# Optimization experiments

Hardware: AMD Instinct MI355X
Metric: run time of the kernel (lower is better)

Reference implementation:

```python
import jax, jax.numpy as jnp
import numpy as np

DIM = 768
HEADS = 12
HEAD_DIM = DIM // HEADS
SCALE = HEAD_DIM ** -0.5
LN_EPS = 1e-5


def setup_inputs() -> dict:
    key = jax.random.key(0)
    ks = jax.random.split(key, 12)
    B, N, C = 8, 1024, DIM
    g = (6.0 / (C + 3 * C)) ** 0.5  # xavier_uniform bound for qkv
    gp = (6.0 / (C + C)) ** 0.5     # xavier_uniform bound for proj
    return {
        "x": jax.random.normal(ks[0], (B, N, C), jnp.float32),
        "w_qkv_id": jax.random.uniform(ks[1], (3 * C, C), jnp.float32, -g, g),
        "w_qkv_cloth": jax.random.uniform(ks[2], (3 * C, C), jnp.float32, -g, g),
        "w_proj_id": jax.random.uniform(ks[3], (C, C), jnp.float32, -gp, gp),
        "b_proj_id": jnp.zeros((C,), jnp.float32),
        "w_proj_cloth": jax.random.uniform(ks[4], (C, C), jnp.float32, -gp, gp),
        "b_proj_cloth": jnp.zeros((C,), jnp.float32),
        "ln_id_w": jnp.ones((C,), jnp.float32),
        "ln_id_b": jnp.zeros((C,), jnp.float32),
        "ln_cloth_w": jnp.ones((C,), jnp.float32),
        "ln_cloth_b": jnp.zeros((C,), jnp.float32),
        "orth_scale": jnp.asarray(0.1, jnp.float32),
    }


def _layernorm(x, w, b):
    mu = jnp.mean(x, axis=-1, keepdims=True)
    var = jnp.var(x, axis=-1, keepdims=True)
    return (x - mu) * jax.lax.rsqrt(var + LN_EPS) * w + b


def _split_heads(qkv, B, N):
    qkv = qkv.reshape(B, N, 3, HEADS, HEAD_DIM).transpose(2, 0, 3, 1, 4)
    return qkv[0], qkv[1], qkv[2]


def _attn(q, k, v):
    s = jnp.einsum("bhnd,bhmd->bhnm", q, k) * SCALE
    s = jnp.clip(s, -20.0, 20.0)
    a = jax.nn.softmax(s, axis=-1)
    a = jnp.where(jnp.isnan(a), jnp.zeros_like(a), a)  # nan guard (dropout = eval/identity)
    return jnp.einsum("bhnm,bhmd->bhnd", a, v)


def reference(x, w_qkv_id, w_qkv_cloth, w_proj_id, b_proj_id, w_proj_cloth,
              b_proj_cloth, ln_id_w, ln_id_b, ln_cloth_w, ln_cloth_b, orth_scale):
    B, N, C = x.shape
    q_id, k_id, v_id = _split_heads(x @ w_qkv_id.T, B, N)
    q_cl, k_cl, v_cl = _split_heads(x @ w_qkv_cloth.T, B, N)

    # Gram-Schmidt orthogonal projection of q_id against q_cloth
    dot = jnp.sum(q_id * q_cl, axis=-1, keepdims=True)          # [B,H,N,1]
    norm_sq = jnp.sum(q_cl * q_cl, axis=-1, keepdims=True) + 1e-5
    coeff = jnp.clip(dot / norm_sq, -1.0, 1.0)
    scale = jnp.clip(orth_scale, 0.0, 1.0)
    q_id_ortho = q_id - scale * (coeff * q_cl)
    saliency = jnp.clip(jnp.mean(jnp.abs(dot) / jnp.sqrt(norm_sq), axis=1), 0.0, 1.0)  # [B,N,1]

    out_id = _attn(q_id_ortho, k_id, v_id).transpose(0, 2, 1, 3).reshape(B, N, C)
    out_cl = _attn(q_cl, k_cl, v_cl).transpose(0, 2, 1, 3).reshape(B, N, C)

    id_feat = _layernorm(out_id @ w_proj_id.T + b_proj_id, ln_id_w, ln_id_b)
    cl_feat = _layernorm(out_cl @ w_proj_cloth.T + b_proj_cloth, ln_cloth_w, ln_cloth_b)
    return id_feat, cl_feat, saliency
```

## Files before the change

### kernel.cpp

```cpp
#include <hip/hip_runtime.h>

typedef unsigned short u16;
typedef short s16x8 __attribute__((ext_vector_type(8)));
typedef float f32x4 __attribute__((ext_vector_type(4)));

#define DEV __device__ __forceinline__

#if __has_builtin(__builtin_amdgcn_exp2f)
#define EXP2F(x) __builtin_amdgcn_exp2f(x)
#else
#define EXP2F(x) exp2f(x)
#endif

DEV u16 f2bf(float f) {
  unsigned int u = __float_as_uint(f);
  u = (u + 0x7fffu + ((u >> 16) & 1u)) >> 16;
  return (u16)u;
}
DEV float bf2f(u16 h) { return __uint_as_float(((unsigned int)h) << 16); }
DEV unsigned int pk_trunc(float lo, float hi) {
  return __builtin_amdgcn_perm(__float_as_uint(hi), __float_as_uint(lo), 0x07060302u);
}

DEV void g2l16(const void* g, void* l) {
  __builtin_amdgcn_global_load_lds(
      (const __attribute__((address_space(1))) unsigned int*)g,
      (__attribute__((address_space(3))) unsigned int*)l, 16, 0, 0);
}

#define SPLANE 6291456

#define BAR __builtin_amdgcn_s_barrier()
#define WAIT_VM(n) asm volatile("s_waitcnt vmcnt(" #n ")" ::: "memory")
#define WAIT_LGKM0 asm volatile("s_waitcnt lgkmcnt(0)" ::: "memory")
#define PRIO1 __builtin_amdgcn_s_setprio(1)
#define PRIO0 __builtin_amdgcn_s_setprio(0)

__global__ __launch_bounds__(256) void k_cvt(const float* __restrict__ x,
                                             const float* __restrict__ wqi,
                                             const float* __restrict__ wqc,
                                             const float* __restrict__ wpi,
                                             const float* __restrict__ wpc,
                                             u16* __restrict__ xb,
                                             u16* __restrict__ wqkv,
                                             u16* __restrict__ wproj) {
  int i = blockIdx.x * 256 + threadIdx.x;
  const float* src; u16* dst; int off;
  if (i < 1572864)      { src = x;   dst = xb;             off = 0; }
  else if (i < 2015232) { src = wqi; dst = wqkv;           off = 1572864; }
  else if (i < 2457600) { src = wqc; dst = wqkv + 1769472; off = 2015232; }
  else if (i < 2605056) { src = wpi; dst = wproj;          off = 2457600; }
  else                  { src = wpc; dst = wproj + 589824; off = 2605056; }
  int j = i - off;
  float4 v = ((const float4*)src)[j];
  ushort4 o;
  o.x = f2bf(v.x); o.y = f2bf(v.y); o.z = f2bf(v.z); o.w = f2bf(v.w);
  ((ushort4*)dst)[j] = o;
}


DEV void qstg(const u16* pX, const u16* pW, int koff, u16* lA, u16* lB, int wave) {
#pragma unroll
  for (int it = 0; it < 4; ++it) {
    int rb = wave * 32 + it * 8;
    g2l16(pX + koff + it * (8 * 768), &lA[rb * 64]);
    g2l16(pW + koff + it * (8 * 768), &lB[rb * 64]);
  }
}

DEV void qcomp(const u16* lA, const u16* lB, int wr, int wc, int fr, int fq,
               f32x4 (&acc)[4][4]) {
#pragma unroll
  for (int ks = 0; ks < 2; ++ks) {
    s16x8 af[4], bfr[4];
#pragma unroll
    for (int i = 0; i < 4; i++) {
      int row = wc + i * 16 + fr;
      af[i] = *(const s16x8*)&lB[row * 64 + (((ks * 4 + fq) ^ (row & 7)) * 8)];
    }
#pragma unroll
    for (int j = 0; j < 4; j++) {
      int row = wr + j * 16 + fr;
      bfr[j] = *(const s16x8*)&lA[row * 64 + (((ks * 4 + fq) ^ (row & 7)) * 8)];
    }
    PRIO1;
#pragma unroll
    for (int i = 0; i < 4; i++)
#pragma unroll
      for (int j = 0; j < 4; j++)
        acc[i][j] = __builtin_amdgcn_mfma_f32_16x16x32_bf16(af[i], bfr[j], acc[i][j], 0, 0, 0);
    PRIO0;
  }
}

__global__ __launch_bounds__(256, 2) void k_qkv_gemm(const u16* __restrict__ X,
                                                     const u16* __restrict__ Wq,
                                                     u16* __restrict__ QK,
                                                     u16* __restrict__ VT,
                                                     float* __restrict__ sal) {
  __shared__ __align__(16) u16 sm[32768];

  const int idx = blockIdx.x;
  const int tid = threadIdx.x;
  if (idx < 32) sal[idx * 256 + tid] = 0.f;

  const int swz = (idx & 7) * 288 + (idx >> 3);
  const int bx = swz % 18;
  const int rem = swz / 18;
  const int by = rem & 63;
  const int z = rem >> 6;
  const int n0 = bx * 128, m0 = by * 128;

  const int wave = tid >> 6, lane = tid & 63;
  const int wr = (wave >> 1) * 64, wc = (wave & 1) * 64;
  const int fr = lane & 15, fq = lane >> 4;

  const int srow = lane >> 3;
  const int scol = ((lane & 7) ^ srow) * 8;

  const u16* pX = X + (size_t)(m0 + wave * 32 + srow) * 768 + scol;
  const u16* pW = Wq + (size_t)z * (2304 * 768) + (size_t)(n0 + wave * 32 + srow) * 768 + scol;

  u16* const lA0 = sm;
  u16* const lB0 = sm + 8192;
  u16* const lA1 = sm + 16384;
  u16* const lB1 = sm + 24576;

  f32x4 acc[4][4];
#pragma unroll
  for (int i = 0; i < 4; i++)
#pragma unroll
    for (int j = 0; j < 4; j++) acc[i][j] = (f32x4){0.f, 0.f, 0.f, 0.f};

  qstg(pX, pW, 0, lA0, lB0, wave);
  qstg(pX, pW, 64, lA1, lB1, wave);
  WAIT_VM(8);
  BAR;

  const u16* pX2 = pX + 128;
  const u16* pW2 = pW + 128;

#pragma unroll
  for (int ii = 0; ii < 6; ++ii) {
    qcomp(lA0, lB0, wr, wc, fr, fq, acc);
    BAR;
    if (ii < 5) {
      qstg(pX2, pW2, 0, lA0, lB0, wave);
      WAIT_VM(8);
    } else {
      WAIT_VM(0);
    }
    BAR;
    qcomp(lA1, lB1, wr, wc, fr, fq, acc);
    BAR;
    if (ii < 5) {
      qstg(pX2, pW2, 64, lA1, lB1, wave);
      WAIT_VM(8);
      pX2 += 128; pW2 += 128;
    }
    BAR;
  }

  __syncthreads();
  const int c0 = n0 + wc;
  const int t0 = m0 + wr;
  const int b = t0 >> 10, tt0 = t0 & 1023;
  if (c0 < 1536) {
    u16* ep = sm + wave * 4608;
#pragma unroll
    for (int i = 0; i < 4; i++)
#pragma unroll
      for (int j = 0; j < 4; j++) {
        unsigned int lo = (unsigned int)f2bf(acc[i][j][0]) | ((unsigned int)f2bf(acc[i][j][1]) << 16);
        unsigned int hi = (unsigned int)f2bf(acc[i][j][2]) | ((unsigned int)f2bf(acc[i][j][3]) << 16);
        uint2 pk; pk.x = lo; pk.y = hi;
        *(uint2*)&ep[(j * 16 + fr) * 72 + i * 16 + fq * 4] = pk;
      }
    __builtin_amdgcn_s_waitcnt(0);
    const int three = (c0 >= 768) ? 1 : 0;
    const int h = (c0 - three * 768) >> 6;
    u16* dst = QK + ((size_t)z * 2 + three) * SPLANE +
               ((size_t)(b * 12 + h) * 1024 + tt0) * 64;
#pragma unroll
    for (int pass = 0; pass < 8; ++pass) {
      int row = pass * 8 + (lane >> 3);
      int dch = (lane & 7) * 8;
      *(uint4*)&dst[(size_t)row * 64 + dch] = *(const uint4*)&ep[row * 72 + dch];
    }
  } else {
    const int h = (c0 - 1536) >> 6;
    u16* dst = VT + (size_t)z * SPLANE + ((size_t)(b * 12 + h) * 64) * 1024 + tt0;
    u16* ep2 = sm + wave * 5632;
#pragma unroll
    for (int i = 0; i < 4; i++)
#pragma unroll
      for (int j = 0; j < 4; j++)
#pragma unroll
        for (int r = 0; r < 4; r++)
          ep2[(i * 16 + fq * 4 + r) * 88 + j * 16 + fr] = f2bf(acc[i][j][r]);
    __builtin_amdgcn_s_waitcnt(0);
#pragma unroll
    for (int pass = 0; pass < 8; ++pass) {
      int d = pass * 8 + (lane >> 3);
      int tch = (lane & 7) * 8;
      *(uint4*)&dst[(size_t)d * 1024 + tch] = *(const uint4*)&ep2[d * 88 + tch];
    }
  }
}

#define AST 72
#define PST 40
__global__ __launch_bounds__(256, 3) void k_attn(const u16* __restrict__ QK,
                                                 const u16* __restrict__ VT,
                                                 const float* __restrict__ orth_scale,
                                                 float* __restrict__ sal,
                                                 u16* __restrict__ aout) {
  __shared__ __align__(16) u16 sm[19456];
  u16* lK = sm;
  u16* lVT = sm + 4608;
  const int lid = blockIdx.x;
  const int swz = (lid & 7) * 96 + (lid >> 3);
  const int qb = swz & 3;
  const int pr = swz >> 2;
  const int z = pr / 96, bh = pr - (pr / 96) * 96;
  const int q0 = qb * 256;
  const int b = bh / 12, hd = bh - b * 12;
  const size_t plane = (size_t)bh * 65536;
  const u16* Q  = QK + (size_t)z * 2 * SPLANE + plane;
  const u16* K  = QK + ((size_t)z * 2 + 1) * SPLANE + plane;
  const u16* Vt = VT + (size_t)z * SPLANE + plane;

  const int tid = threadIdx.x, wave = tid >> 6, lane = tid & 63;
  const int fr = lane & 15, fq = lane >> 4;
  u16* lP = sm + 9216 + wave * 2560;

  s16x8 qf[4][2];
#pragma unroll
  for (int s = 0; s < 4; s++) {
    const u16* qrow = Q + (size_t)(q0 + wave * 64 + s * 16 + fr) * 64;
    qf[s][0] = *(const s16x8*)&qrow[fq * 8];
    qf[s][1] = *(const s16x8*)&qrow[32 + fq * 8];
  }

  if (z == 0) {
    const float scale = fminf(fmaxf(orth_scale[0], 0.f), 1.f);
    const u16* Qc = QK + (size_t)2 * SPLANE + plane;
#pragma unroll
    for (int s = 0; s < 4; s++) {
      const u16* qcrow = Qc + (size_t)(q0 + wave * 64 + s * 16 + fr) * 64;
      s16x8 qc0 = *(const s16x8*)&qcrow[fq * 8];
      s16x8 qc1 = *(const s16x8*)&qcrow[32 + fq * 8];
      float d = 0.f, nq = 0.f;
#pragma unroll
      for (int e = 0; e < 8; e++) {
        float a0 = bf2f((u16)qf[s][0][e]), a1 = bf2f((u16)qf[s][1][e]);
        float c0 = bf2f((u16)qc0[e]),      c1 = bf2f((u16)qc1[e]);
        d  = fmaf(a0, c0, fmaf(a1, c1, d));
        nq = fmaf(c0, c0, fmaf(c1, c1, nq));
      }
      d += __shfl_xor(d, 16);  d += __shfl_xor(d, 32);
      nq += __shfl_xor(nq, 16); nq += __shfl_xor(nq, 32);
      nq += 1e-5f;
      float coeff = fminf(fmaxf(d / nq, -1.f), 1.f);
      float sc = scale * coeff;
#pragma unroll
      for (int e = 0; e < 8; e++) {
        qf[s][0][e] = (short)f2bf(bf2f((u16)qf[s][0][e]) - sc * bf2f((u16)qc0[e]));
        qf[s][1][e] = (short)f2bf(bf2f((u16)qf[s][1][e]) - sc * bf2f((u16)qc1[e]));
      }
      if (lane < 16)
        atomicAdd(&sal[b * 1024 + q0 + wave * 64 + s * 16 + fr], fabsf(d) / sqrtf(nq));
    }
  }

  f32x4 oacc[4][4];
  float lsum[4];
#pragma unroll
  for (int s = 0; s < 4; s++) {
    lsum[s] = 0.f;
#pragma unroll
    for (int j = 0; j < 4; j++) oacc[s][j] = (f32x4){0.f, 0.f, 0.f, 0.f};
  }

  const int srow = tid >> 3, sc8 = (tid & 7) * 8;

  uint4 rk0 = *(const uint4*)&K[(size_t)srow * 64 + sc8];
  uint4 rk1 = *(const uint4*)&K[(size_t)(srow + 32) * 64 + sc8];
  uint4 rv0 = *(const uint4*)&Vt[(size_t)srow * 1024 + sc8];
  uint4 rv1 = *(const uint4*)&Vt[(size_t)(srow + 32) * 1024 + sc8];

  for (int kv0 = 0; kv0 < 1024; kv0 += 64) {
    __syncthreads();
    *(uint4*)&lK[srow * AST + sc8]         = rk0;
    *(uint4*)&lK[(srow + 32) * AST + sc8]  = rk1;
    *(uint4*)&lVT[srow * AST + sc8]        = rv0;
    *(uint4*)&lVT[(srow + 32) * AST + sc8] = rv1;
    __syncthreads();

    {
      int nxt = (kv0 + 64) & 1023;
      const u16* kb = K + (size_t)nxt * 64;
      rk0 = *(const uint4*)&kb[(size_t)srow * 64 + sc8];
      rk1 = *(const uint4*)&kb[(size_t)(srow + 32) * 64 + sc8];
      const u16* vb = Vt + nxt;
      rv0 = *(const uint4*)&vb[(size_t)srow * 1024 + sc8];
      rv1 = *(const uint4*)&vb[(size_t)(srow + 32) * 1024 + sc8];
    }

#pragma unroll
    for (int ph = 0; ph < 2; ++ph) {
#pragma unroll
      for (int jh = 0; jh < 2; ++jh) {
        const int jt = ph * 2 + jh;
        s16x8 kf0 = *(const s16x8*)&lK[(jt * 16 + fr) * AST + fq * 8];
        s16x8 kf1 = *(const s16x8*)&lK[(jt * 16 + fr) * AST + 32 + fq * 8];
#pragma unroll
        for (int s = 0; s < 4; s++) {
          f32x4 t = (f32x4){0.f, 0.f, 0.f, 0.f};
          t = __builtin_amdgcn_mfma_f32_16x16x32_bf16(kf0, qf[s][0], t, 0, 0, 0);
          t = __builtin_amdgcn_mfma_f32_16x16x32_bf16(kf1, qf[s][1], t, 0, 0, 0);
          float p0 = EXP2F(fmaf(t[0], 0.18033688f, -28.8539008f));
          float p1 = EXP2F(fmaf(t[1], 0.18033688f, -28.8539008f));
          float p2 = EXP2F(fmaf(t[2], 0.18033688f, -28.8539008f));
          float p3 = EXP2F(fmaf(t[3], 0.18033688f, -28.8539008f));
          lsum[s] += (p0 + p1) + (p2 + p3);
          uint2 pk; pk.x = pk_trunc(p0, p1); pk.y = pk_trunc(p2, p3);
          *(uint2*)&lP[(s * 16 + fr) * PST + jh * 16 + fq * 4] = pk;
        }
      }
      WAIT_LGKM0;
      s16x8 pa[4];
#pragma unroll
      for (int s = 0; s < 4; s++) pa[s] = *(const s16x8*)&lP[(s * 16 + fr) * PST + fq * 8];
#pragma unroll
      for (int jt = 0; jt < 4; jt++) {
        s16x8 vb = *(const s16x8*)&lVT[(jt * 16 + fr) * AST + ph * 32 + fq * 8];
#pragma unroll
        for (int s = 0; s < 4; s++)
          oacc[s][jt] = __builtin_amdgcn_mfma_f32_16x16x32_bf16(pa[s], vb, oacc[s][jt], 0, 0, 0);
      }
    }
  }

#pragma unroll
  for (int s = 0; s < 4; s++) {
    float v = lsum[s];
    v += __shfl_xor(v, 16);
    v += __shfl_xor(v, 32);
    lsum[s] = v;
  }
#pragma unroll
  for (int s = 0; s < 4; s++) {
#pragma unroll
    for (int r = 0; r < 4; r++) {
      float inv = 1.f / __shfl(lsum[s], fq * 4 + r);
      int t = q0 + wave * 64 + s * 16 + fq * 4 + r;
      size_t base = ((size_t)z * 8192 + b * 1024 + t) * 768 + hd * 64 + fr;
#pragma unroll
      for (int jt = 0; jt < 4; jt++)
        aout[base + jt * 16] = f2bf(oacc[s][jt][r] * inv);
    }
  }
}

__global__ __launch_bounds__(256) void k_proj_gemm(const u16* __restrict__ A,
                                                   const u16* __restrict__ Wp,
                                                   const float* __restrict__ bias_id,
                                                   const float* __restrict__ bias_cl,
                                                   float* __restrict__ sal,
                                                   u16* __restrict__ out) {
  __shared__ __align__(16) u16 sm[18432];
  u16* lA = sm;
  u16* lB = sm + 8192;
  const int idx = blockIdx.x;
  const int tid = threadIdx.x;
  if (idx < 32) {
    int i2 = idx * 256 + tid;
    float v = sal[i2] * (1.f / 12.f);
    sal[i2] = fminf(fmaxf(v, 0.f), 1.f);
  }
  const int swz = (idx & 7) * 96 + (idx >> 3);
  const int bx = swz % 6;
  const int rem = swz / 6;
  const int by = rem & 63;
  const int z = rem >> 6;
  const int n0 = bx * 128, m0 = by * 128;
  const u16* Az = A + (size_t)z * 8192 * 768;
  const u16* Wz = Wp + (size_t)z * 768 * 768;
  const float* bias = z ? bias_cl : bias_id;
  u16* oz = out + (size_t)z * 8192 * 768;
  const int wave = tid >> 6, lane = tid & 63;
  const int wr = (wave >> 1) * 64, wc = (wave & 1) * 64;
  const int fr = lane & 15, fq = lane >> 4;

  float bv[4][4];
#pragma unroll
  for (int i = 0; i < 4; i++)
#pragma unroll
    for (int r = 0; r < 4; r++) bv[i][r] = bias[n0 + wc + i * 16 + fq * 4 + r];

  f32x4 acc[4][4];
#pragma unroll
  for (int i = 0; i < 4; i++)
#pragma unroll
    for (int j = 0; j < 4; j++) acc[i][j] = (f32x4){0.f, 0.f, 0.f, 0.f};

  const int srow = lane >> 3;
  const int scol = ((lane & 7) ^ srow) * 8;

  const u16* pAz = Az + (size_t)(m0 + wave * 32 + srow) * 768 + scol;
  const u16* pWz = Wz + (size_t)(n0 + wave * 32 + srow) * 768 + scol;

  for (int k0 = 0; k0 < 768; k0 += 64) {
    __syncthreads();
#pragma unroll
    for (int it = 0; it < 4; ++it) {
      int rb = wave * 32 + it * 8;
      g2l16(pAz + it * (8 * 768) + k0, &lA[rb * 64]);
      g2l16(pWz + it * (8 * 768) + k0, &lB[rb * 64]);
    }
    __syncthreads();
#pragma unroll
    for (int ks = 0; ks < 2; ++ks) {
      s16x8 af[4], bfr[4];
#pragma unroll
      for (int i = 0; i < 4; i++) {
        int row = wc + i * 16 + fr;
        af[i] = *(const s16x8*)&lB[row * 64 + (((ks * 4 + fq) ^ (row & 7)) * 8)];
      }
#pragma unroll
      for (int j = 0; j < 4; j++) {
        int row = wr + j * 16 + fr;
        bfr[j] = *(const s16x8*)&lA[row * 64 + (((ks * 4 + fq) ^ (row & 7)) * 8)];
      }
#pragma unroll
      for (int i = 0; i < 4; i++)
#pragma unroll
        for (int j = 0; j < 4; j++)
          acc[i][j] = __builtin_amdgcn_mfma_f32_16x16x32_bf16(af[i], bfr[j], acc[i][j], 0, 0, 0);
    }
  }

  __syncthreads();
  u16* ep = sm + wave * 4608;
#pragma unroll
  for (int i = 0; i < 4; i++)
#pragma unroll
    for (int j = 0; j < 4; j++) {
      unsigned int lo = (unsigned int)f2bf(acc[i][j][0] + bv[i][0]) |
                        ((unsigned int)f2bf(acc[i][j][1] + bv[i][1]) << 16);
      unsigned int hi = (unsigned int)f2bf(acc[i][j][2] + bv[i][2]) |
                        ((unsigned int)f2bf(acc[i][j][3] + bv[i][3]) << 16);
      uint2 pk; pk.x = lo; pk.y = hi;
      *(uint2*)&ep[(j * 16 + fr) * 72 + i * 16 + fq * 4] = pk;
    }
  __builtin_amdgcn_s_waitcnt(0);

  const int c0 = n0 + wc;
#pragma unroll
  for (int pass = 0; pass < 8; ++pass) {
    int row = pass * 8 + (lane >> 3);
    int dch = (lane & 7) * 8;
    u16* dst = oz + (size_t)(m0 + wr + row) * 768 + c0;
    *(uint4*)&dst[dch] = *(const uint4*)&ep[row * 72 + dch];
  }
}

__global__ __launch_bounds__(256) void k_ln(const u16* __restrict__ pin,
                                            const float* __restrict__ w_id,
                                            const float* __restrict__ b_id,
                                            const float* __restrict__ w_cl,
                                            const float* __restrict__ b_cl,
                                            float* __restrict__ out) {
  __shared__ float red[2][8];
  const int row = blockIdx.x;
  const int z = row >> 13;
  const float* w = z ? w_cl : w_id;
  const float* bb = z ? b_cl : b_id;
  const u16* x = pin + (size_t)row * 768;
  float v[3];
  float s = 0.f, s2 = 0.f;
#pragma unroll
  for (int i = 0; i < 3; i++) {
    v[i] = bf2f(x[threadIdx.x + i * 256]);
    s += v[i];
    s2 += v[i] * v[i];
  }
#pragma unroll
  for (int sh = 1; sh < 64; sh <<= 1) { s += __shfl_xor(s, sh); s2 += __shfl_xor(s2, sh); }
  const int wave = threadIdx.x >> 6, lane = threadIdx.x & 63;
  if (lane == 0) { red[0][wave] = s; red[1][wave] = s2; }
  __syncthreads();
  s = red[0][0] + red[0][1] + red[0][2] + red[0][3];
  s2 = red[1][0] + red[1][1] + red[1][2] + red[1][3];
  float mu = s * (1.f / 768.f);
  float var = s2 * (1.f / 768.f) - mu * mu;
  float rstd = rsqrtf(fmaxf(var, 0.f) + 1e-5f);
  float* o = out + (size_t)row * 768;
#pragma unroll
  for (int i = 0; i < 3; i++) {
    int c = threadIdx.x + i * 256;
    o[c] = (v[i] - mu) * rstd * w[c] + bb[c];
  }
}

extern "C" void kernel_launch(void* const* d_in, const int* in_sizes, int n_in,
                              void* d_out, int out_size, void* d_ws, size_t ws_size,
                              hipStream_t stream) {
  const float* x        = (const float*)d_in[0];
  const float* w_qkv_id = (const float*)d_in[1];
  const float* w_qkv_cl = (const float*)d_in[2];
  const float* w_proj_id= (const float*)d_in[3];
  const float* b_proj_id= (const float*)d_in[4];
  const float* w_proj_cl= (const float*)d_in[5];
  const float* b_proj_cl= (const float*)d_in[6];
  const float* ln_id_w  = (const float*)d_in[7];
  const float* ln_id_b  = (const float*)d_in[8];
  const float* ln_cl_w  = (const float*)d_in[9];
  const float* ln_cl_b  = (const float*)d_in[10];
  const float* orth     = (const float*)d_in[11];
  float* out = (float*)d_out;
  float* sal = out + 12582912;

  u16* xb    = (u16*)d_ws;
  u16* wqkv  = xb + 6291456;
  u16* wproj = wqkv + 3538944;
  u16* qk    = wproj + 1179648;
  u16* vt    = qk + 25165824;
  u16* aout  = vt + 12582912;
  u16* pout  = qk;

  k_cvt<<<10752, 256, 0, stream>>>(x, w_qkv_id, w_qkv_cl, w_proj_id, w_proj_cl,
                                   xb, wqkv, wproj);
  k_qkv_gemm<<<2304, 256, 0, stream>>>(xb, wqkv, qk, vt, sal);
  k_attn<<<768, 256, 0, stream>>>(qk, vt, orth, sal, aout);
  k_proj_gemm<<<768, 256, 0, stream>>>(aout, wproj, b_proj_id, b_proj_cl, sal, pout);
  k_ln<<<16384, 256, 0, stream>>>(pout, ln_id_w, ln_id_b, ln_cl_w, ln_cl_b, out);
}
```

Before: 279.1 us.

## Double-buffer K/V tiles via direct global-to-LDS loads with XOR swizzle

Replaces the register-staged K/V prefetch with direct global-to-LDS async loads (g2l16) into two LDS buffers, issuing tile t+2 while tile t is computed. The unpadded 64-wide LDS rows use an XOR swizzle instead of padding to avoid bank conflicts, and s_setprio hints are wrapped around the MFMA sections. The aim is to hide global load latency and free the registers used for staging. In exchange LDS use grows from about 38KB to 52KB per block, which may limit how many blocks fit per CU.

```diff
diff --git a/kernel.cpp b/kernel.cpp
--- a/kernel.cpp
+++ b/kernel.cpp
@@ -208,16 +208,13 @@
   }
 }
 
-#define AST 72
 #define PST 40
 __global__ __launch_bounds__(256, 3) void k_attn(const u16* __restrict__ QK,
                                                  const u16* __restrict__ VT,
                                                  const float* __restrict__ orth_scale,
                                                  float* __restrict__ sal,
                                                  u16* __restrict__ aout) {
-  __shared__ __align__(16) u16 sm[19456];
-  u16* lK = sm;
-  u16* lVT = sm + 4608;
+  __shared__ __align__(16) u16 sm[26624];
   const int lid = blockIdx.x;
   const int swz = (lid & 7) * 96 + (lid >> 3);
   const int qb = swz & 3;
@@ -232,7 +229,7 @@
 
   const int tid = threadIdx.x, wave = tid >> 6, lane = tid & 63;
   const int fr = lane & 15, fq = lane >> 4;
-  u16* lP = sm + 9216 + wave * 2560;
+  u16* lP = sm + 16384 + wave * 2560;
 
   s16x8 qf[4][2];
 #pragma unroll
@@ -282,64 +279,84 @@
     for (int j = 0; j < 4; j++) oacc[s][j] = (f32x4){0.f, 0.f, 0.f, 0.f};
   }
 
-  const int srow = tid >> 3, sc8 = (tid & 7) * 8;
-
-  uint4 rk0 = *(const uint4*)&K[(size_t)srow * 64 + sc8];
-  uint4 rk1 = *(const uint4*)&K[(size_t)(srow + 32) * 64 + sc8];
-  uint4 rv0 = *(const uint4*)&Vt[(size_t)srow * 1024 + sc8];
-  uint4 rv1 = *(const uint4*)&Vt[(size_t)(srow + 32) * 1024 + sc8];
-
-  for (int kv0 = 0; kv0 < 1024; kv0 += 64) {
-    __syncthreads();
-    *(uint4*)&lK[srow * AST + sc8]         = rk0;
-    *(uint4*)&lK[(srow + 32) * AST + sc8]  = rk1;
-    *(uint4*)&lVT[srow * AST + sc8]        = rv0;
-    *(uint4*)&lVT[(srow + 32) * AST + sc8] = rv1;
-    __syncthreads();
-
-    {
-      int nxt = (kv0 + 64) & 1023;
-      const u16* kb = K + (size_t)nxt * 64;
-      rk0 = *(const uint4*)&kb[(size_t)srow * 64 + sc8];
-      rk1 = *(const uint4*)&kb[(size_t)(srow + 32) * 64 + sc8];
-      const u16* vb = Vt + nxt;
-      rv0 = *(const uint4*)&vb[(size_t)srow * 1024 + sc8];
-      rv1 = *(const uint4*)&vb[(size_t)(srow + 32) * 1024 + sc8];
-    }
+  const int r8 = lane >> 3;
+  const int csrc = ((lane & 7) ^ r8) * 8;
+  const u16* pK = K + (size_t)(wave * 8 + r8) * 64 + csrc;
+  const u16* pV = Vt + (size_t)(wave * 8 + r8) * 1024 + csrc;
+
+  {
+    u16* bK = sm;            u16* bV = sm + 4096;
+    g2l16(pK,          bK + wave * 512);
+    g2l16(pK + 2048,   bK + 2048 + wave * 512);
+    g2l16(pV,          bV + wave * 512);
+    g2l16(pV + 32768,  bV + 2048 + wave * 512);
+    bK = sm + 8192;          bV = sm + 12288;
+    g2l16(pK + 4096,         bK + wave * 512);
+    g2l16(pK + 4096 + 2048,  bK + 2048 + wave * 512);
+    g2l16(pV + 64,           bV + wave * 512);
+    g2l16(pV + 64 + 32768,   bV + 2048 + wave * 512);
+  }
+  WAIT_VM(4);
+  BAR;
+
+  for (int t = 0; t < 16; ++t) {
+    const int cb = (t & 1) * 8192;
+    const u16* lK  = sm + cb;
+    const u16* lVT = sm + cb + 4096;
 
 #pragma unroll
     for (int ph = 0; ph < 2; ++ph) {
 #pragma unroll
       for (int jh = 0; jh < 2; ++jh) {
         const int jt = ph * 2 + jh;
-        s16x8 kf0 = *(const s16x8*)&lK[(jt * 16 + fr) * AST + fq * 8];
-        s16x8 kf1 = *(const s16x8*)&lK[(jt * 16 + fr) * AST + 32 + fq * 8];
+        const int krow = (jt * 16 + fr) * 64;
+        s16x8 kf0 = *(const s16x8*)&lK[krow + ((fq ^ (fr & 7)) * 8)];
+        s16x8 kf1 = *(const s16x8*)&lK[krow + (((fq + 4) ^ (fr & 7)) * 8)];
+        PRIO1;
 #pragma unroll
         for (int s = 0; s < 4; s++) {
-          f32x4 t = (f32x4){0.f, 0.f, 0.f, 0.f};
-          t = __builtin_amdgcn_mfma_f32_16x16x32_bf16(kf0, qf[s][0], t, 0, 0, 0);
-          t = __builtin_amdgcn_mfma_f32_16x16x32_bf16(kf1, qf[s][1], t, 0, 0, 0);
-          float p0 = EXP2F(fmaf(t[0], 0.18033688f, -28.8539008f));
-          float p1 = EXP2F(fmaf(t[1], 0.18033688f, -28.8539008f));
-          float p2 = EXP2F(fmaf(t[2], 0.18033688f, -28.8539008f));
-          float p3 = EXP2F(fmaf(t[3], 0.18033688f, -28.8539008f));
+          f32x4 t2 = (f32x4){0.f, 0.f, 0.f, 0.f};
+          t2 = __builtin_amdgcn_mfma_f32_16x16x32_bf16(kf0, qf[s][0], t2, 0, 0, 0);
+          t2 = __builtin_amdgcn_mfma_f32_16x16x32_bf16(kf1, qf[s][1], t2, 0, 0, 0);
+          float p0 = EXP2F(fmaf(t2[0], 0.18033688f, -28.8539008f));
+          float p1 = EXP2F(fmaf(t2[1], 0.18033688f, -28.8539008f));
+          float p2 = EXP2F(fmaf(t2[2], 0.18033688f, -28.8539008f));
+          float p3 = EXP2F(fmaf(t2[3], 0.18033688f, -28.8539008f));
           lsum[s] += (p0 + p1) + (p2 + p3);
           uint2 pk; pk.x = pk_trunc(p0, p1); pk.y = pk_trunc(p2, p3);
           *(uint2*)&lP[(s * 16 + fr) * PST + jh * 16 + fq * 4] = pk;
         }
+        PRIO0;
       }
       WAIT_LGKM0;
       s16x8 pa[4];
 #pragma unroll
       for (int s = 0; s < 4; s++) pa[s] = *(const s16x8*)&lP[(s * 16 + fr) * PST + fq * 8];
+      PRIO1;
 #pragma unroll
       for (int jt = 0; jt < 4; jt++) {
-        s16x8 vb = *(const s16x8*)&lVT[(jt * 16 + fr) * AST + ph * 32 + fq * 8];
+        s16x8 vb = *(const s16x8*)&lVT[(jt * 16 + fr) * 64 + (((ph * 4 + fq) ^ (fr & 7)) * 8)];
 #pragma unroll
         for (int s = 0; s < 4; s++)
           oacc[s][jt] = __builtin_amdgcn_mfma_f32_16x16x32_bf16(pa[s], vb, oacc[s][jt], 0, 0, 0);
       }
-    }
+      PRIO0;
+    }
+
+    BAR;
+    if (t < 14) {
+      u16* bK = sm + cb;  u16* bV = sm + cb + 4096;
+      const u16* nK = pK + (size_t)(t + 2) * 4096;
+      const u16* nV = pV + (size_t)(t + 2) * 64;
+      g2l16(nK,          bK + wave * 512);
+      g2l16(nK + 2048,   bK + 2048 + wave * 512);
+      g2l16(nV,          bV + wave * 512);
+      g2l16(nV + 32768,  bV + 2048 + wave * 512);
+      WAIT_VM(4);
+    } else if (t == 14) {
+      WAIT_VM(0);
+    }
+    BAR;
   }
 
 #pragma unroll
```

Result: slower. 347.8 us (+24.6%).
